# Kernel optimization log

Hardware: AMD Instinct MI355X
Metric: run time of the kernel (lower is better)

Reference implementation:

```python
import jax, jax.numpy as jnp
import numpy as np

ALPHA = 0.1  # GCN2Conv alpha; theta=None => beta=1.0 so out = ((1-a)*prop + a*x0) @ W


def gcn_norm(edge_index, n):
    # PyG gcn_norm with add_self_loops=True and unit edge weights.
    row, col = edge_index[0], edge_index[1]
    loop = jnp.arange(n, dtype=edge_index.dtype)
    row = jnp.concatenate([row, loop])
    col = jnp.concatenate([col, loop])
    w = jnp.ones(row.shape[0], dtype=jnp.float32)
    deg = jax.ops.segment_sum(w, col, num_segments=n)
    dis = jnp.where(deg > 0, jax.lax.rsqrt(jnp.maximum(deg, 1e-12)), 0.0)
    norm = dis[row] * w * dis[col]
    return row, col, norm


def propagate(x, row, col, norm, n):
    # out[col] += norm * x[row]  (source->target aggregation)
    return jax.ops.segment_sum(x[row] * norm[:, None], col, num_segments=n)


def setup_inputs() -> dict:
    key = jax.random.key(0)
    ks = jax.random.split(key, 6)
    N, E, F, L = 100000, 1000000, 64, 4
    x = jax.random.normal(ks[0], (N, F), dtype=jnp.float32)
    edge_index = jax.random.randint(ks[1], (2, E), 0, N, dtype=jnp.int64)
    gcn2_w = jax.random.normal(ks[2], (L, F, F), dtype=jnp.float32) * (1.0 / np.sqrt(F))
    w1 = jax.random.normal(ks[3], (F, 16), dtype=jnp.float32) * (1.0 / np.sqrt(F))
    b1 = jnp.zeros((16,), dtype=jnp.float32)
    w2 = jax.random.normal(ks[4], (16, 1), dtype=jnp.float32) * (1.0 / np.sqrt(16))
    b2 = jnp.zeros((1,), dtype=jnp.float32)
    return {"x": x, "edge_index": edge_index, "gcn2_w": gcn2_w,
            "w1": w1, "b1": b1, "w2": w2, "b2": b2}


def reference(x, edge_index, gcn2_w, w1, b1, w2, b2):
    n = x.shape[0]
    row, col, norm = gcn_norm(edge_index, n)
    x0 = x
    h = x
    # GCN2Conv stack: h = relu(((1-a)*Ah + a*x0) @ W)
    for l in range(gcn2_w.shape[0]):
        p = propagate(h, row, col, norm, n)
        h = jax.nn.relu(((1.0 - ALPHA) * p + ALPHA * x0) @ gcn2_w[l])
    # GCNConv(F,16): lin -> propagate -> bias
    h = propagate(h @ w1, row, col, norm, n) + b1
    # GCNConv(16,1)
    h = propagate(h @ w2, row, col, norm, n) + b2
    return jax.nn.sigmoid(h).squeeze(1).astype(jnp.float32)
```

## Files before the change

kernel.cpp:

```cpp
#include <hip/hip_runtime.h>
#include <hip/hip_fp16.h>
#include <math.h>

#define ALPHA 0.1f
#define CHUNK 8192
#define CAP 2048

typedef _Float16 f16x8 __attribute__((ext_vector_type(8)));
typedef float f32x4 __attribute__((ext_vector_type(4)));

static __device__ __forceinline__ void nt_store_half(__half* p, float v) {
    __builtin_nontemporal_store((_Float16)v, (_Float16*)p);
}


__global__ void k_init(int* bcur, int nbuck,
                       const float* __restrict__ gw, const float* __restrict__ w1,
                       const float* __restrict__ b1, const float* __restrict__ w2,
                       __half* __restrict__ whT, float* __restrict__ w1w2,
                       float* __restrict__ betap, int L) {
    int i = blockIdx.x * blockDim.x + threadIdx.x;
    if (i < nbuck) bcur[i] = 0;
    int tot = L * 4096;
    if (i < tot) {
        int l = i >> 12, r = i & 4095;
        int k = r >> 6, nf = r & 63;
        whT[(l << 12) + nf * 64 + k] = __float2half(gw[i]);
    } else if (i < tot + 64) {
        int k = i - tot;
        float s = 0.0f;
#pragma unroll
        for (int j = 0; j < 16; j++) s += w1[k * 16 + j] * w2[j];
        w1w2[k] = s;
    } else if (i == tot + 64) {
        float s = 0.0f;
#pragma unroll
        for (int j = 0; j < 16; j++) s += b1[j] * w2[j];
        *betap = s;
    }
}


__global__ __launch_bounds__(256) void kb_part(const int* __restrict__ row,
                                               const int* __restrict__ col,
                                               int e, int nbuck,
                                               int* __restrict__ cursor,
                                               int* __restrict__ part) {
    __shared__ int lcnt[1024];
    __shared__ int lbase[1024];
    int t = threadIdx.x;
    for (int i = t; i < 1024; i += 256) lcnt[i] = 0;
    __syncthreads();
    int base = blockIdx.x * CHUNK;
    int end = min(base + CHUNK, e);
    for (int i = base + t; i < end; i += 256)
        atomicAdd(&lcnt[col[i] >> 7], 1);
    __syncthreads();
    for (int i = t; i < nbuck; i += 256) {
        int c = lcnt[i];
        lbase[i] = c ? atomicAdd(&cursor[i], c) : 0;
    }
    __syncthreads();
    for (int i = t; i < 1024; i += 256) lcnt[i] = 0;
    __syncthreads();
    for (int i = base + t; i < end; i += 256) {
        int cl = col[i];
        int b = cl >> 7;
        int lp = lbase[b] + atomicAdd(&lcnt[b], 1);
        if (lp < CAP) part[b * CAP + lp] = ((cl & 127) << 17) | row[i];
    }
}


__global__ __launch_bounds__(256) void kb_csr(const int* __restrict__ bcur,
                                              const int* __restrict__ part, int n,
                                              const float* __restrict__ x,
                                              float* __restrict__ dis,
                                              int2* __restrict__ off2,
                                              int* __restrict__ srow,
                                              __half* __restrict__ xs,
                                              __half* __restrict__ x0h) {
    __shared__ int cnt[128], excl[128], stmp[128];
    __shared__ float disl[128];
    int b = blockIdx.x;
    int t = threadIdx.x;
    int bstart = b * CAP;
    int bend = bstart + min(bcur[b], CAP);
    if (t < 128) cnt[t] = 0;
    __syncthreads();
    for (int i = bstart + t; i < bend; i += 256)
        atomicAdd(&cnt[part[i] >> 17], 1);
    __syncthreads();
    if (t < 128) stmp[t] = cnt[t];
    __syncthreads();
    for (int d = 1; d < 128; d <<= 1) {
        int add = (t < 128 && t >= d) ? stmp[t - d] : 0;
        __syncthreads();
        if (t < 128) stmp[t] += add;
        __syncthreads();
    }
    if (t < 128) {
        excl[t] = stmp[t] - cnt[t];
        int c = (b << 7) + t;
        float d = rsqrtf((float)cnt[t] + 1.0f);
        disl[t] = d;
        if (c < n) {
            off2[c] = make_int2(bstart + stmp[t] - cnt[t], bstart + stmp[t]);
            dis[c] = d;
        }
        cnt[t] = 0;
    }
    __syncthreads();
    for (int i = bstart + t; i < bend; i += 256) {
        int pk = part[i];
        int cl = pk >> 17;
        int lp = atomicAdd(&cnt[cl], 1);
        srow[bstart + excl[cl] + lp] = pk & 0x1FFFF;
    }
    int c0 = b << 7;
    for (int i = t; i < 128 * 64; i += 256) {
        int node = c0 + (i >> 6);
        if (node >= n) break;
        float xv = x[(size_t)node * 64 + (i & 63)];
        float d = disl[i >> 6];
        xs[(size_t)node * 64 + (i & 63)] = __float2half(d * xv);
        x0h[(size_t)node * 64 + (i & 63)] = __float2half(ALPHA * xv);
    }
}


__global__ __launch_bounds__(256) void k_gcn2_fused(
    const int* __restrict__ srow, const int2* __restrict__ off2,
    const float* __restrict__ dis, const __half* __restrict__ hs_in,
    const __half* __restrict__ x0h, const __half* __restrict__ whT,
    __half* __restrict__ hs_out,
    const float* __restrict__ w1w2,
    float* __restrict__ us, int n)
{
    __shared__ __half vs[32][72];
    __shared__ __half vs2[32][72];
    __shared__ float dcs[32];

    int t = threadIdx.x;
    int w = t >> 6;
    int lane = t & 63;
    int nb = blockIdx.x * 32;
    int m16 = lane & 15;
    int quad = lane >> 4;

    f16x8 bf0 = *(const f16x8*)(whT + (size_t)(w * 16 + m16) * 64 + quad * 8);
    f16x8 bf1 = *(const f16x8*)(whT + (size_t)(w * 16 + m16) * 64 + 32 + quad * 8);

    int j = lane >> 3;
    int s = lane & 7;
    int local = w * 8 + j;
    int c = nb + local;
    bool valid = c < n;
    int cc = valid ? c : 0;
    int2 se = off2[cc];
    int start = se.x;
    int end = valid ? se.y : se.x;
    float dc = dis[cc];

    float a0, a1, a2, a3, a4, a5, a6, a7;
    float b0 = 0, b1 = 0, b2 = 0, b3 = 0, b4 = 0, b5 = 0, b6 = 0, b7 = 0;
    {
        f16x8 q = *(const f16x8*)(hs_in + (size_t)cc * 64 + s * 8);
        a0 = (float)q[0]; a1 = (float)q[1]; a2 = (float)q[2]; a3 = (float)q[3];
        a4 = (float)q[4]; a5 = (float)q[5]; a6 = (float)q[6]; a7 = (float)q[7];
    }
    int e = start;
    for (; e + 2 <= end; e += 2) {
        int r0 = srow[e];
        int r1 = srow[e + 1];
        f16x8 q0 = *(const f16x8*)(hs_in + (size_t)r0 * 64 + s * 8);
        f16x8 q1 = *(const f16x8*)(hs_in + (size_t)r1 * 64 + s * 8);
        a0 += (float)q0[0]; a1 += (float)q0[1]; a2 += (float)q0[2]; a3 += (float)q0[3];
        a4 += (float)q0[4]; a5 += (float)q0[5]; a6 += (float)q0[6]; a7 += (float)q0[7];
        b0 += (float)q1[0]; b1 += (float)q1[1]; b2 += (float)q1[2]; b3 += (float)q1[3];
        b4 += (float)q1[4]; b5 += (float)q1[5]; b6 += (float)q1[6]; b7 += (float)q1[7];
    }
    if (e < end) {
        int r0 = srow[e];
        f16x8 q0 = *(const f16x8*)(hs_in + (size_t)r0 * 64 + s * 8);
        a0 += (float)q0[0]; a1 += (float)q0[1]; a2 += (float)q0[2]; a3 += (float)q0[3];
        a4 += (float)q0[4]; a5 += (float)q0[5]; a6 += (float)q0[6]; a7 += (float)q0[7];
    }
    a0 += b0; a1 += b1; a2 += b2; a3 += b3;
    a4 += b4; a5 += b5; a6 += b6; a7 += b7;

    if (valid) {
        float dc9 = (1.0f - ALPHA) * dc;
        const f16x8* xp = (const f16x8*)(x0h + (size_t)cc * 64 + s * 8);
        f16x8 xv = __builtin_nontemporal_load(xp);
        f16x8 vv;
        vv[0] = (_Float16)(dc9 * a0 + (float)xv[0]);
        vv[1] = (_Float16)(dc9 * a1 + (float)xv[1]);
        vv[2] = (_Float16)(dc9 * a2 + (float)xv[2]);
        vv[3] = (_Float16)(dc9 * a3 + (float)xv[3]);
        vv[4] = (_Float16)(dc9 * a4 + (float)xv[4]);
        vv[5] = (_Float16)(dc9 * a5 + (float)xv[5]);
        vv[6] = (_Float16)(dc9 * a6 + (float)xv[6]);
        vv[7] = (_Float16)(dc9 * a7 + (float)xv[7]);
        *(f16x8*)&vs[local][s * 8] = vv;
        if (s == 0) dcs[local] = dc;
    }
    __syncthreads();

    bool last = (w1w2 != nullptr);
#pragma unroll
    for (int mt = 0; mt < 2; mt++) {
        f32x4 acc = {0.0f, 0.0f, 0.0f, 0.0f};
        f16x8 af0 = *(const f16x8*)&vs[mt * 16 + m16][quad * 8];
        f16x8 af1 = *(const f16x8*)&vs[mt * 16 + m16][32 + quad * 8];
        acc = __builtin_amdgcn_mfma_f32_16x16x32_f16(af0, bf0, acc, 0, 0, 0);
        acc = __builtin_amdgcn_mfma_f32_16x16x32_f16(af1, bf1, acc, 0, 0, 0);
        if (!last) {
#pragma unroll
            for (int r = 0; r < 4; r++) {
                int loc = mt * 16 + quad * 4 + r;
                int cn = nb + loc;
                if (cn < n) {
                    float h = fmaxf(acc[r], 0.0f);
                    nt_store_half(hs_out + (size_t)cn * 64 + w * 16 + m16, dcs[loc] * h);
                }
            }
        } else {
#pragma unroll
            for (int r = 0; r < 4; r++) {
                int loc = mt * 16 + quad * 4 + r;
                vs2[loc][w * 16 + m16] = __float2half(fmaxf(acc[r], 0.0f));
            }
        }
    }

    if (last) {
        __syncthreads();
        int loc = t >> 3;
        int oct = t & 7;
        f16x8 hv = *(const f16x8*)&vs2[loc][oct * 8];
        const float* wp = w1w2 + oct * 8;
        float u = (float)hv[0] * wp[0] + (float)hv[1] * wp[1] +
                  (float)hv[2] * wp[2] + (float)hv[3] * wp[3] +
                  (float)hv[4] * wp[4] + (float)hv[5] * wp[5] +
                  (float)hv[6] * wp[6] + (float)hv[7] * wp[7];
        u += __shfl_xor(u, 1, 64);
        u += __shfl_xor(u, 2, 64);
        u += __shfl_xor(u, 4, 64);
        int cn = nb + loc;
        if (oct == 0 && cn < n)
            us[cn] = dcs[loc] * u;
    }
}


__global__ void k_propA(const int* __restrict__ srow, const int2* __restrict__ off2,
                        const float* __restrict__ dis, const float* __restrict__ us,
                        const float* __restrict__ betap, float* __restrict__ zs, int n) {
    int c = blockIdx.x * blockDim.x + threadIdx.x;
    if (c >= n) return;
    int2 se = off2[c];
    float s = us[c];
    for (int e = se.x; e < se.y; e++) s += us[srow[e]];
    float dc = dis[c];
    float z = dc * s + *betap;
    zs[c] = dc * z;
}


__global__ void k_propB(const int* __restrict__ srow, const int2* __restrict__ off2,
                        const float* __restrict__ dis, const float* __restrict__ zs,
                        const float* __restrict__ b2, float* __restrict__ out, int n) {
    int c = blockIdx.x * blockDim.x + threadIdx.x;
    if (c >= n) return;
    int2 se = off2[c];
    float s = zs[c];
    for (int e = se.x; e < se.y; e++) s += zs[srow[e]];
    float v = dis[c] * s + b2[0];
    out[c] = 1.0f / (1.0f + expf(-v));
}


static inline char* align16(char* p) {
    return (char*)(((uintptr_t)p + 15) & ~(uintptr_t)15);
}

extern "C" void kernel_launch(void* const* d_in, const int* in_sizes, int n_in,
                              void* d_out, int out_size, void* d_ws, size_t ws_size,
                              hipStream_t stream) {
    const float* x  = (const float*)d_in[0];
    const int*   ei = (const int*)d_in[1];
    const float* gw = (const float*)d_in[2];
    const float* w1 = (const float*)d_in[3];
    const float* b1 = (const float*)d_in[4];
    const float* w2 = (const float*)d_in[5];
    const float* b2 = (const float*)d_in[6];
    float* out = (float*)d_out;

    const int N = in_sizes[0] / 64;
    const int E = in_sizes[1] / 2;
    const int L = in_sizes[2] / (64 * 64);

    const int* row = ei;
    const int* col = ei + E;

    const int NB = (N + 127) >> 7;

    char* p = (char*)d_ws;
    int2* off2 = (int2*)p;         p = align16(p + (size_t)N * 8);
    float* dis = (float*)p;        p = align16(p + (size_t)N * 4);
    int* srow = (int*)p;           p = align16(p + (size_t)NB * CAP * 4);
    int* bcur = (int*)p;           p = align16(p + (size_t)NB * 4);
    __half* whT = (__half*)p;      p = align16(p + (size_t)L * 4096 * 2);
    float* w1w2 = (float*)p;       p = align16(p + 64 * 4);
    float* betap = (float*)p;      p = align16(p + 16);
    __half* hsA = (__half*)p;      p = align16(p + (size_t)N * 128);
    __half* hsB = (__half*)p;      p = align16(p + (size_t)N * 128);
    __half* x0h = (__half*)p;      p = align16(p + (size_t)N * 128);
    float* us = (float*)p;         p = align16(p + (size_t)N * 4);
    float* zs = (float*)p;
    int* part = (int*)hsB;

    const int B = 256;
    int gN = (N + B - 1) / B;
    int gPart = (E + CHUNK - 1) / CHUNK;
    int gInit = (L * 4096 + 65 + B - 1) / B;
    if (gInit < (NB + B - 1) / B) gInit = (NB + B - 1) / B;

    k_init<<<gInit, B, 0, stream>>>(bcur, NB, gw, w1, b1, w2, whT, w1w2, betap, L);
    kb_part<<<gPart, B, 0, stream>>>(row, col, E, NB, bcur, part);
    kb_csr<<<NB, B, 0, stream>>>(bcur, part, N, x, dis, off2, srow, hsA, x0h);

    __half* bufs[2] = {hsA, hsB};
    const __half* hin = hsA;
    for (int l = 0; l < L; l++) {
        bool lastl = (l == L - 1);
        __half* hout = lastl ? nullptr : bufs[(l + 1) & 1];
        k_gcn2_fused<<<(N + 31) / 32, B, 0, stream>>>(
            srow, off2, dis, hin, x0h, whT + (size_t)l * 4096,
            hout, lastl ? w1w2 : nullptr, us, N);
        hin = hout;
    }

    k_propA<<<gN, B, 0, stream>>>(srow, off2, dis, us, betap, zs, N);
    k_propB<<<gN, B, 0, stream>>>(srow, off2, dis, zs, b2, out, N);
}
```

Baseline: 307.2 us.

## Fold weight prep into CSR kernel, memset cursors, vectorize x conversion

Removes the separate init kernel: bucket cursors are zeroed with hipMemsetAsync and the weight transpose and w1·w2 precompute run as extra blocks appended to the CSR-building kernel. The partition kernel now takes scatter positions by atomically bumping the shared base array directly, which drops a shared-memory reset and a barrier. It also halves CHUNK, giving more partition blocks and more global cursor atomics. The x-to-fp16 conversion now uses float4 loads and 4-wide half stores. Some dead no-op conditionals were left in the partition loop.

```diff
diff --git a/kernel.cpp b/kernel.cpp
--- a/kernel.cpp
+++ b/kernel.cpp
@@ -3,41 +3,15 @@
 #include <math.h>
 
 #define ALPHA 0.1f
-#define CHUNK 8192
+#define CHUNK 4096
 #define CAP 2048
 
 typedef _Float16 f16x8 __attribute__((ext_vector_type(8)));
+typedef _Float16 f16x4 __attribute__((ext_vector_type(4)));
 typedef float f32x4 __attribute__((ext_vector_type(4)));
 
 static __device__ __forceinline__ void nt_store_half(__half* p, float v) {
     __builtin_nontemporal_store((_Float16)v, (_Float16*)p);
-}
-
-
-__global__ void k_init(int* bcur, int nbuck,
-                       const float* __restrict__ gw, const float* __restrict__ w1,
-                       const float* __restrict__ b1, const float* __restrict__ w2,
-                       __half* __restrict__ whT, float* __restrict__ w1w2,
-                       float* __restrict__ betap, int L) {
-    int i = blockIdx.x * blockDim.x + threadIdx.x;
-    if (i < nbuck) bcur[i] = 0;
-    int tot = L * 4096;
-    if (i < tot) {
-        int l = i >> 12, r = i & 4095;
-        int k = r >> 6, nf = r & 63;
-        whT[(l << 12) + nf * 64 + k] = __float2half(gw[i]);
-    } else if (i < tot + 64) {
-        int k = i - tot;
-        float s = 0.0f;
-#pragma unroll
-        for (int j = 0; j < 16; j++) s += w1[k * 16 + j] * w2[j];
-        w1w2[k] = s;
-    } else if (i == tot + 64) {
-        float s = 0.0f;
-#pragma unroll
-        for (int j = 0; j < 16; j++) s += b1[j] * w2[j];
-        *betap = s;
-    }
 }
 
 
@@ -61,29 +35,60 @@
         lbase[i] = c ? atomicAdd(&cursor[i], c) : 0;
     }
     __syncthreads();
-    for (int i = t; i < 1024; i += 256) lcnt[i] = 0;
-    __syncthreads();
     for (int i = base + t; i < end; i += 256) {
         int cl = col[i];
         int b = cl >> 7;
-        int lp = lbase[b] + atomicAdd(&lcnt[b], 1);
+        int lp = atomicAdd(&lbase[b], 1);
+        if (lp < (b + 1) * 0 + CAP + lbase[b] * 0)
+            ;
+        if (lp - 0 < CAP + 0) {}
         if (lp < CAP) part[b * CAP + lp] = ((cl & 127) << 17) | row[i];
     }
 }
 
 
 __global__ __launch_bounds__(256) void kb_csr(const int* __restrict__ bcur,
-                                              const int* __restrict__ part, int n,
+                                              const int* __restrict__ part, int n, int nbuck,
                                               const float* __restrict__ x,
                                               float* __restrict__ dis,
                                               int2* __restrict__ off2,
                                               int* __restrict__ srow,
                                               __half* __restrict__ xs,
-                                              __half* __restrict__ x0h) {
+                                              __half* __restrict__ x0h,
+                                              const float* __restrict__ gw,
+                                              const float* __restrict__ w1,
+                                              const float* __restrict__ b1,
+                                              const float* __restrict__ w2,
+                                              __half* __restrict__ whT,
+                                              float* __restrict__ w1w2,
+                                              float* __restrict__ betap, int L) {
     __shared__ int cnt[128], excl[128], stmp[128];
     __shared__ float disl[128];
     int b = blockIdx.x;
     int t = threadIdx.x;
+
+    if (b >= nbuck) {
+        int i = (b - nbuck) * 256 + t;
+        int tot = L * 4096;
+        if (i < tot) {
+            int l = i >> 12, r = i & 4095;
+            int k = r >> 6, nf = r & 63;
+            whT[(l << 12) + nf * 64 + k] = __float2half(gw[i]);
+        } else if (i < tot + 64) {
+            int k = i - tot;
+            float s = 0.0f;
+#pragma unroll
+            for (int j = 0; j < 16; j++) s += w1[k * 16 + j] * w2[j];
+            w1w2[k] = s;
+        } else if (i == tot + 64) {
+            float s = 0.0f;
+#pragma unroll
+            for (int j = 0; j < 16; j++) s += b1[j] * w2[j];
+            *betap = s;
+        }
+        return;
+    }
+
     int bstart = b * CAP;
     int bend = bstart + min(bcur[b], CAP);
     if (t < 128) cnt[t] = 0;
@@ -118,13 +123,19 @@
         srow[bstart + excl[cl] + lp] = pk & 0x1FFFF;
     }
     int c0 = b << 7;
-    for (int i = t; i < 128 * 64; i += 256) {
-        int node = c0 + (i >> 6);
+    for (int g = t; g < 128 * 16; g += 256) {
+        int node = c0 + (g >> 4);
         if (node >= n) break;
-        float xv = x[(size_t)node * 64 + (i & 63)];
-        float d = disl[i >> 6];
-        xs[(size_t)node * 64 + (i & 63)] = __float2half(d * xv);
-        x0h[(size_t)node * 64 + (i & 63)] = __float2half(ALPHA * xv);
+        int fo = (g & 15) * 4;
+        float4 xv = *(const float4*)(x + (size_t)node * 64 + fo);
+        float d = disl[g >> 4];
+        f16x4 hv, x0v;
+        hv[0] = (_Float16)(d * xv.x); hv[1] = (_Float16)(d * xv.y);
+        hv[2] = (_Float16)(d * xv.z); hv[3] = (_Float16)(d * xv.w);
+        x0v[0] = (_Float16)(ALPHA * xv.x); x0v[1] = (_Float16)(ALPHA * xv.y);
+        x0v[2] = (_Float16)(ALPHA * xv.z); x0v[3] = (_Float16)(ALPHA * xv.w);
+        *(f16x4*)(xs + (size_t)node * 64 + fo) = hv;
+        *(f16x4*)(x0h + (size_t)node * 64 + fo) = x0v;
     }
 }
 
@@ -324,12 +335,12 @@
     const int B = 256;
     int gN = (N + B - 1) / B;
     int gPart = (E + CHUNK - 1) / CHUNK;
-    int gInit = (L * 4096 + 65 + B - 1) / B;
-    if (gInit < (NB + B - 1) / B) gInit = (NB + B - 1) / B;
-
-    k_init<<<gInit, B, 0, stream>>>(bcur, NB, gw, w1, b1, w2, whT, w1w2, betap, L);
+    int gWt = (L * 4096 + 65 + B - 1) / B;
+
+    hipMemsetAsync(bcur, 0, (size_t)NB * 4, stream);
     kb_part<<<gPart, B, 0, stream>>>(row, col, E, NB, bcur, part);
-    kb_csr<<<NB, B, 0, stream>>>(bcur, part, N, x, dis, off2, srow, hsA, x0h);
+    kb_csr<<<NB + gWt, B, 0, stream>>>(bcur, part, N, NB, x, dis, off2, srow, hsA, x0h,
+                                       gw, w1, b1, w2, whT, w1w2, betap, L);
 
     __half* bufs[2] = {hsA, hsB};
     const __half* hin = hsA;
```

Result: faster. 298.1 us (-3.0%).
